# Kernel optimization log

Hardware: AMD Instinct MI355X
Metric: run time of the kernel (lower is better)

## Reference

```python
import jax, jax.numpy as jnp
import numpy as np


def setup_inputs() -> dict:
    key = jax.random.key(0)
    ks = jax.random.split(key, 4)
    B, T, D, H, E = 4, 2048, 1024, 4096, 8
    s = 0.02
    x = jax.random.normal(ks[0], (B, T, D), dtype=jnp.float32)
    Wr = jax.random.normal(ks[1], (D, E), dtype=jnp.float32) * s
    br = jnp.zeros((E,), dtype=jnp.float32)
    W1 = jax.random.normal(ks[2], (E, D, H), dtype=jnp.float32) * s
    b1 = jnp.zeros((E, H), dtype=jnp.float32)
    W2 = jax.random.normal(ks[3], (E, H, D), dtype=jnp.float32) * s
    b2 = jnp.zeros((E, D), dtype=jnp.float32)
    return {"x": x, "Wr": Wr, "br": br, "W1": W1, "b1": b1, "W2": W2, "b2": b2}


def reference(x, Wr, br, W1, b1, W2, b2):
    # Router: top-1 selection
    logits = jnp.einsum('btd,de->bte', x, Wr) + br            # [B,T,E]
    probs = jax.nn.softmax(logits, axis=-1)                   # [B,T,E]
    expert_idx = jnp.argmax(probs, axis=-1)                   # [B,T] int
    E = W1.shape[0]
    onehot = jax.nn.one_hot(expert_idx, E, dtype=x.dtype)     # [B,T,E]
    # Dense grouped-MLP over all experts, then combine with one-hot routing.
    # h: [B,E,T,H]
    h = jax.nn.relu(jnp.einsum('btd,edh->beth', x, W1) + b1[None, :, None, :])
    y = jnp.einsum('beth,ehd->betd', h, W2) + b2[None, :, None, :]  # [B,E,T,D]
    out = jnp.einsum('bte,betd->btd', onehot, y)              # [B,T,D]
    return out, probs, expert_idx
```

## Files before the change

kernel.cpp:

```cpp
#include <hip/hip_runtime.h>

#define NTOK 8192
#define DD 1024
#define HH 4096
#define EE 8
#define MAXBLK 72
#define NT1 16
#define NT2 64

typedef __attribute__((ext_vector_type(8))) short bf16x8;
typedef __attribute__((ext_vector_type(4))) float f32x4;

__device__ __forceinline__ unsigned short f2bf(float f) {
  unsigned u = __builtin_bit_cast(unsigned, f);
  u += 0x7fffu + ((u >> 16) & 1u);
  return (unsigned short)(u >> 16);
}

union Pack8 {
  unsigned short u[8];
  uint4 v;
};

__device__ __forceinline__ void gload_lds16(const void* g, void* l) {
  __builtin_amdgcn_global_load_lds(
      (const __attribute__((address_space(1))) unsigned int*)g,
      (__attribute__((address_space(3))) unsigned int*)l, 16, 0, 0);
}

__global__ __launch_bounds__(256) void k_router(
    const float* __restrict__ x, const float* __restrict__ Wr,
    const float* __restrict__ br, float* __restrict__ probs,
    float* __restrict__ idxf, int* __restrict__ idxi,
    unsigned short* __restrict__ xb) {
  const int lane = threadIdx.x & 63;
  const int token = blockIdx.x * 4 + (threadIdx.x >> 6);
  const float* xr = x + (size_t)token * DD;

  float acc[EE];
#pragma unroll
  for (int e = 0; e < EE; ++e) acc[e] = 0.f;

#pragma unroll
  for (int i = 0; i < 4; ++i) {
    const int d0 = i * 256 + lane * 4;
    const float4 xv = *reinterpret_cast<const float4*>(xr + d0);
    union { unsigned short u[4]; uint2 v; } pk;
    pk.u[0] = f2bf(xv.x); pk.u[1] = f2bf(xv.y);
    pk.u[2] = f2bf(xv.z); pk.u[3] = f2bf(xv.w);
    *reinterpret_cast<uint2*>(xb + (size_t)token * DD + d0) = pk.v;
    const float xs[4] = {xv.x, xv.y, xv.z, xv.w};
#pragma unroll
    for (int j = 0; j < 4; ++j) {
      const float xd = xs[j];
      const float4 w0 = *reinterpret_cast<const float4*>(Wr + (size_t)(d0 + j) * EE);
      const float4 w1 = *reinterpret_cast<const float4*>(Wr + (size_t)(d0 + j) * EE + 4);
      acc[0] += xd * w0.x; acc[1] += xd * w0.y; acc[2] += xd * w0.z; acc[3] += xd * w0.w;
      acc[4] += xd * w1.x; acc[5] += xd * w1.y; acc[6] += xd * w1.z; acc[7] += xd * w1.w;
    }
  }
#pragma unroll
  for (int s = 32; s > 0; s >>= 1) {
#pragma unroll
    for (int e = 0; e < EE; ++e) acc[e] += __shfl_xor(acc[e], s, 64);
  }

  float lg[EE];
#pragma unroll
  for (int e = 0; e < EE; ++e) lg[e] = acc[e] + br[e];

  int best = 0;
  float bv = lg[0];
#pragma unroll
  for (int e = 1; e < EE; ++e) {
    if (lg[e] > bv) { bv = lg[e]; best = e; }
  }
  float p[EE], s = 0.f;
#pragma unroll
  for (int e = 0; e < EE; ++e) { p[e] = expf(lg[e] - bv); s += p[e]; }
  const float inv = 1.f / s;

  if (lane == 0) {
#pragma unroll
    for (int e = 0; e < EE; ++e) probs[(size_t)token * EE + e] = p[e] * inv;
    idxf[token] = (float)best;
    idxi[token] = best;
  }
}

__global__ __launch_bounds__(512) void k_compact(const int* __restrict__ idxi,
                                                 int* __restrict__ cnt,
                                                 int* __restrict__ off,
                                                 int* __restrict__ sorted,
                                                 int* __restrict__ meta) {
  __shared__ int sidx[NTOK];
  __shared__ int scnt[EE], soff[EE];
  const int tid = threadIdx.x;
  for (int i = tid; i < NTOK; i += 512) sidx[i] = idxi[i];
  __syncthreads();
  const int w = tid >> 6, lane = tid & 63;
  if (w < EE) {
    int c = 0;
    for (int i = 0; i < NTOK / 64; ++i) {
      unsigned long long m = __ballot(sidx[i * 64 + lane] == w);
      c += __popcll(m);
    }
    if (lane == 0) scnt[w] = c;
  }
  __syncthreads();
  if (tid == 0) {
    int s = 0;
    for (int e = 0; e < EE; ++e) { soff[e] = s; s += scnt[e]; }
    int nb = 0;
    for (int e = 0; e < EE; ++e) {
      const int nmb = (scnt[e] + 127) >> 7;
      for (int m = 0; m < nmb; ++m) {
        meta[16 + nb] = e;
        meta[96 + nb] = m << 7;
        ++nb;
      }
    }
    meta[0] = nb;
  }
  __syncthreads();
  if (w < EE) {
    int base = soff[w];
    const unsigned long long ltmask = (1ull << lane) - 1ull;
    for (int i = 0; i < NTOK / 64; ++i) {
      const int tok = i * 64 + lane;
      const bool f = (sidx[tok] == w);
      unsigned long long m = __ballot(f);
      if (f) {
        int r = __popcll(m & ltmask);
        sorted[base + r] = tok;
      }
      base += __popcll(m);
    }
    if (lane == 0) { cnt[w] = scnt[w]; off[w] = soff[w]; }
  }
}

__global__ __launch_bounds__(256) void k_trcvt64(const float* __restrict__ in,
                                                 unsigned short* __restrict__ outp,
                                                 int R, int C) {
  const int e = blockIdx.z;
  const int r0 = blockIdx.y * 64, c0 = blockIdx.x * 64;
  const float* src = in + (size_t)e * R * C + (size_t)r0 * C + c0;
  unsigned short* dst = outp + (size_t)e * R * C + (size_t)c0 * R + r0;
  __shared__ unsigned short t[64 * 66];
  const int tid = threadIdx.x;
#pragma unroll
  for (int it = 0; it < 4; ++it) {
    const int r = it * 16 + (tid >> 4), c4 = (tid & 15) * 4;
    const float4 v = *reinterpret_cast<const float4*>(src + (size_t)r * C + c4);
    t[r * 66 + c4 + 0] = f2bf(v.x);
    t[r * 66 + c4 + 1] = f2bf(v.y);
    t[r * 66 + c4 + 2] = f2bf(v.z);
    t[r * 66 + c4 + 3] = f2bf(v.w);
  }
  __syncthreads();
#pragma unroll
  for (int it = 0; it < 2; ++it) {
    const int cc = it * 32 + (tid >> 3), r8 = (tid & 7) * 8;
    Pack8 p;
#pragma unroll
    for (int j = 0; j < 8; ++j) p.u[j] = t[(r8 + j) * 66 + cc];
    *reinterpret_cast<uint4*>(dst + (size_t)cc * R + r8) = p.v;
  }
}

__global__ __launch_bounds__(256) void k_gemm1n(
    const unsigned short* __restrict__ xb, const unsigned short* __restrict__ W1t,
    const float* __restrict__ b1, const int* __restrict__ meta,
    const int* __restrict__ cnt, const int* __restrict__ off,
    const int* __restrict__ sorted, unsigned short* __restrict__ h) {
  const int bid = blockIdx.x;
  if (bid >= meta[0]) return;
  const int e = meta[16 + bid];
  const int m0 = meta[96 + bid];
  const int c = cnt[e], base = off[e];
  const int n0 = blockIdx.y * 128;

  __shared__ __align__(16) unsigned short Al[2][128 * 64];
  __shared__ __align__(16) unsigned short Bl[2][128 * 64];

  const int tid = threadIdx.x, l = tid & 63, w = tid >> 6;

  const unsigned short* aptr[4];
  const unsigned short* bptr[4];
  int soff4[4];
#pragma unroll
  for (int i = 0; i < 4; ++i) {
    const int r = i * 32 + w * 8 + (l >> 3);
    const int swz = ((l & 7) ^ (r & 7)) * 8;
    int ar = m0 + r; if (ar >= c) ar = c - 1;
    const int tok = sorted[base + ar];
    aptr[i] = xb + (size_t)tok * DD + swz;
    bptr[i] = W1t + ((size_t)e * HH + n0 + r) * DD + swz;
    soff4[i] = r * 64 + (l & 7) * 8;
  }

  const int lr = l & 15, lg = l >> 4;
  const int wr = w >> 1, wc = w & 1;
  int aoff[4], boff[4], asw[4], bsw[4];
#pragma unroll
  for (int m = 0; m < 4; ++m) {
    int row = wr * 64 + m * 16 + lr;
    aoff[m] = row * 64; asw[m] = row & 7;
    row = wc * 64 + m * 16 + lr;
    boff[m] = row * 64; bsw[m] = row & 7;
  }

  f32x4 acc[4][4];
#pragma unroll
  for (int m = 0; m < 4; ++m)
#pragma unroll
    for (int n = 0; n < 4; ++n) acc[m][n] = {0.f, 0.f, 0.f, 0.f};

#pragma unroll
  for (int i = 0; i < 4; ++i) gload_lds16(aptr[i], &Al[0][soff4[i]]);
#pragma unroll
  for (int i = 0; i < 4; ++i) gload_lds16(bptr[i], &Bl[0][soff4[i]]);

  int cur = 0;
#pragma unroll 1
  for (int t = 0; t < NT1 - 1; ++t) {
    const int kn = (t + 1) * 64;
#pragma unroll
    for (int i = 0; i < 4; ++i) gload_lds16(aptr[i] + kn, &Al[cur ^ 1][soff4[i]]);
    asm volatile("s_waitcnt vmcnt(4)" ::: "memory");
    __builtin_amdgcn_s_barrier();
    {
      bf16x8 af[4], bv[4];
#pragma unroll
      for (int m = 0; m < 4; ++m)
        af[m] = *reinterpret_cast<const bf16x8*>(&Al[cur][aoff[m] + ((lg ^ asw[m]) * 8)]);
#pragma unroll
      for (int n = 0; n < 4; ++n)
        bv[n] = *reinterpret_cast<const bf16x8*>(&Bl[cur][boff[n] + ((lg ^ bsw[n]) * 8)]);
#pragma unroll
      for (int m = 0; m < 4; ++m)
#pragma unroll
        for (int n = 0; n < 4; ++n)
          acc[m][n] = __builtin_amdgcn_mfma_f32_16x16x32_bf16(af[m], bv[n], acc[m][n], 0, 0, 0);
    }
#pragma unroll
    for (int i = 0; i < 4; ++i) gload_lds16(bptr[i] + kn, &Bl[cur ^ 1][soff4[i]]);
    {
      bf16x8 af[4], bv[4];
#pragma unroll
      for (int m = 0; m < 4; ++m)
        af[m] = *reinterpret_cast<const bf16x8*>(&Al[cur][aoff[m] + (((4 + lg) ^ asw[m]) * 8)]);
#pragma unroll
      for (int n = 0; n < 4; ++n)
        bv[n] = *reinterpret_cast<const bf16x8*>(&Bl[cur][boff[n] + (((4 + lg) ^ bsw[n]) * 8)]);
#pragma unroll
      for (int m = 0; m < 4; ++m)
#pragma unroll
        for (int n = 0; n < 4; ++n)
          acc[m][n] = __builtin_amdgcn_mfma_f32_16x16x32_bf16(af[m], bv[n], acc[m][n], 0, 0, 0);
    }
    __builtin_amdgcn_s_barrier();
    cur ^= 1;
  }
  asm volatile("s_waitcnt vmcnt(0)" ::: "memory");
  __builtin_amdgcn_s_barrier();
#pragma unroll
  for (int ks = 0; ks < 2; ++ks) {
    bf16x8 af[4], bv[4];
#pragma unroll
    for (int m = 0; m < 4; ++m)
      af[m] = *reinterpret_cast<const bf16x8*>(&Al[cur][aoff[m] + (((ks * 4 + lg) ^ asw[m]) * 8)]);
#pragma unroll
    for (int n = 0; n < 4; ++n)
      bv[n] = *reinterpret_cast<const bf16x8*>(&Bl[cur][boff[n] + (((ks * 4 + lg) ^ bsw[n]) * 8)]);
#pragma unroll
    for (int m = 0; m < 4; ++m)
#pragma unroll
      for (int n = 0; n < 4; ++n)
        acc[m][n] = __builtin_amdgcn_mfma_f32_16x16x32_bf16(af[m], bv[n], acc[m][n], 0, 0, 0);
  }

  const int valid = c - m0;
#pragma unroll
  for (int m = 0; m < 4; ++m) {
#pragma unroll
    for (int rr = 0; rr < 4; ++rr) {
      const int tr = wr * 64 + m * 16 + lg * 4 + rr;
      if (tr < valid) {
        const size_t row = (size_t)(base + m0 + tr);
#pragma unroll
        for (int n = 0; n < 4; ++n) {
          const int col = n0 + wc * 64 + n * 16 + lr;
          const float v = acc[m][n][rr] + b1[e * HH + col];
          h[row * HH + col] = f2bf(fmaxf(v, 0.f));
        }
      }
    }
  }
}

__global__ __launch_bounds__(256) void k_gemm2n(
    const unsigned short* __restrict__ h, const unsigned short* __restrict__ W2t,
    const float* __restrict__ b2, const int* __restrict__ meta,
    const int* __restrict__ cnt, const int* __restrict__ off,
    const int* __restrict__ sorted, float* __restrict__ out) {
  const int bid = blockIdx.x;
  if (bid >= meta[0]) return;
  const int e = meta[16 + bid];
  const int m0 = meta[96 + bid];
  const int c = cnt[e], base = off[e];
  const int n0 = blockIdx.y * 128;

  __shared__ __align__(16) unsigned short Al[2][128 * 64];
  __shared__ __align__(16) unsigned short Bl[2][128 * 64];

  const int tid = threadIdx.x, l = tid & 63, w = tid >> 6;

  const unsigned short* aptr[4];
  const unsigned short* bptr[4];
  int soff4[4];
#pragma unroll
  for (int i = 0; i < 4; ++i) {
    const int r = i * 32 + w * 8 + (l >> 3);
    const int swz = ((l & 7) ^ (r & 7)) * 8;
    int ar = m0 + r; if (ar >= c) ar = c - 1;
    aptr[i] = h + (size_t)(base + ar) * HH + swz;
    bptr[i] = W2t + ((size_t)e * DD + n0 + r) * HH + swz;
    soff4[i] = r * 64 + (l & 7) * 8;
  }

  const int lr = l & 15, lg = l >> 4;
  const int wr = w >> 1, wc = w & 1;
  int aoff[4], boff[4], asw[4], bsw[4];
#pragma unroll
  for (int m = 0; m < 4; ++m) {
    int row = wr * 64 + m * 16 + lr;
    aoff[m] = row * 64; asw[m] = row & 7;
    row = wc * 64 + m * 16 + lr;
    boff[m] = row * 64; bsw[m] = row & 7;
  }

  f32x4 acc[4][4];
#pragma unroll
  for (int m = 0; m < 4; ++m)
#pragma unroll
    for (int n = 0; n < 4; ++n) acc[m][n] = {0.f, 0.f, 0.f, 0.f};

#pragma unroll
  for (int i = 0; i < 4; ++i) gload_lds16(aptr[i], &Al[0][soff4[i]]);
#pragma unroll
  for (int i = 0; i < 4; ++i) gload_lds16(bptr[i], &Bl[0][soff4[i]]);

  int cur = 0;
#pragma unroll 1
  for (int t = 0; t < NT2 - 1; ++t) {
    const int kn = (t + 1) * 64;
#pragma unroll
    for (int i = 0; i < 4; ++i) gload_lds16(aptr[i] + kn, &Al[cur ^ 1][soff4[i]]);
    asm volatile("s_waitcnt vmcnt(4)" ::: "memory");
    __builtin_amdgcn_s_barrier();
    {
      bf16x8 af[4], bv[4];
#pragma unroll
      for (int m = 0; m < 4; ++m)
        af[m] = *reinterpret_cast<const bf16x8*>(&Al[cur][aoff[m] + ((lg ^ asw[m]) * 8)]);
#pragma unroll
      for (int n = 0; n < 4; ++n)
        bv[n] = *reinterpret_cast<const bf16x8*>(&Bl[cur][boff[n] + ((lg ^ bsw[n]) * 8)]);
#pragma unroll
      for (int m = 0; m < 4; ++m)
#pragma unroll
        for (int n = 0; n < 4; ++n)
          acc[m][n] = __builtin_amdgcn_mfma_f32_16x16x32_bf16(af[m], bv[n], acc[m][n], 0, 0, 0);
    }
#pragma unroll
    for (int i = 0; i < 4; ++i) gload_lds16(bptr[i] + kn, &Bl[cur ^ 1][soff4[i]]);
    {
      bf16x8 af[4], bv[4];
#pragma unroll
      for (int m = 0; m < 4; ++m)
        af[m] = *reinterpret_cast<const bf16x8*>(&Al[cur][aoff[m] + (((4 + lg) ^ asw[m]) * 8)]);
#pragma unroll
      for (int n = 0; n < 4; ++n)
        bv[n] = *reinterpret_cast<const bf16x8*>(&Bl[cur][boff[n] + (((4 + lg) ^ bsw[n]) * 8)]);
#pragma unroll
      for (int m = 0; m < 4; ++m)
#pragma unroll
        for (int n = 0; n < 4; ++n)
          acc[m][n] = __builtin_amdgcn_mfma_f32_16x16x32_bf16(af[m], bv[n], acc[m][n], 0, 0, 0);
    }
    __builtin_amdgcn_s_barrier();
    cur ^= 1;
  }
  asm volatile("s_waitcnt vmcnt(0)" ::: "memory");
  __builtin_amdgcn_s_barrier();
#pragma unroll
  for (int ks = 0; ks < 2; ++ks) {
    bf16x8 af[4], bv[4];
#pragma unroll
    for (int m = 0; m < 4; ++m)
      af[m] = *reinterpret_cast<const bf16x8*>(&Al[cur][aoff[m] + (((ks * 4 + lg) ^ asw[m]) * 8)]);
#pragma unroll
    for (int n = 0; n < 4; ++n)
      bv[n] = *reinterpret_cast<const bf16x8*>(&Bl[cur][boff[n] + (((ks * 4 + lg) ^ bsw[n]) * 8)]);
#pragma unroll
    for (int m = 0; m < 4; ++m)
#pragma unroll
      for (int n = 0; n < 4; ++n)
        acc[m][n] = __builtin_amdgcn_mfma_f32_16x16x32_bf16(af[m], bv[n], acc[m][n], 0, 0, 0);
  }

  const int valid = c - m0;
#pragma unroll
  for (int m = 0; m < 4; ++m) {
#pragma unroll
    for (int rr = 0; rr < 4; ++rr) {
      const int tr = wr * 64 + m * 16 + lg * 4 + rr;
      if (tr < valid) {
        const int token = sorted[base + m0 + tr];
#pragma unroll
        for (int n = 0; n < 4; ++n) {
          const int col = n0 + wc * 64 + n * 16 + lr;
          out[(size_t)token * DD + col] = acc[m][n][rr] + b2[e * DD + col];
        }
      }
    }
  }
}

extern "C" void kernel_launch(void* const* d_in, const int* in_sizes, int n_in,
                              void* d_out, int out_size, void* d_ws, size_t ws_size,
                              hipStream_t stream) {
  const float* x  = (const float*)d_in[0];
  const float* Wr = (const float*)d_in[1];
  const float* br = (const float*)d_in[2];
  const float* W1 = (const float*)d_in[3];
  const float* b1 = (const float*)d_in[4];
  const float* W2 = (const float*)d_in[5];
  const float* b2 = (const float*)d_in[6];

  float* out   = (float*)d_out;
  float* probs = out + (size_t)NTOK * DD;
  float* idxf  = probs + (size_t)NTOK * EE;

  char* ws = (char*)d_ws;
  int* cnt    = (int*)(ws + 0);
  int* off    = (int*)(ws + 64);
  int* meta   = (int*)(ws + 128);
  int* idxi   = (int*)(ws + 1024);
  int* sorted = (int*)(ws + 33792);

  const size_t OFF_XB  = 66560;
  const size_t OFF_W1T = OFF_XB + (size_t)NTOK * DD * 2;
  const size_t OFF_H   = OFF_W1T + (size_t)EE * DD * HH * 2;
  const size_t OFF_W2T = OFF_XB;

  unsigned short* xb  = (unsigned short*)(ws + OFF_XB);
  unsigned short* W1t = (unsigned short*)(ws + OFF_W1T);
  unsigned short* W2t = (unsigned short*)(ws + OFF_W2T);
  unsigned short* h   = (unsigned short*)(ws + OFF_H);

  k_router<<<NTOK / 4, 256, 0, stream>>>(x, Wr, br, probs, idxf, idxi, xb);
  k_compact<<<1, 512, 0, stream>>>(idxi, cnt, off, sorted, meta);
  k_trcvt64<<<dim3(HH / 64, DD / 64, EE), 256, 0, stream>>>(W1, W1t, DD, HH);
  k_gemm1n<<<dim3(MAXBLK, HH / 128), 256, 0, stream>>>(xb, W1t, b1, meta, cnt, off, sorted, h);
  k_trcvt64<<<dim3(DD / 64, HH / 64, EE), 256, 0, stream>>>(W2, W2t, HH, DD);
  k_gemm2n<<<dim3(MAXBLK, DD / 128), 256, 0, stream>>>(h, W2t, b2, meta, cnt, off, sorted, out);
}
```

Before: 412.0 us.

## Split GEMM2 K-dimension across two warp groups and drop double buffering

The second expert GEMM now runs with 512 threads in two warp groups, each covering half of the H reduction with its own LDS tiles. Partial sums are combined through LDS before the output is written. Both GEMMs also drop the async double-buffered pipeline for a simpler single-buffered load, sync, compute loop. The aim is more waves per block on the small GEMM2 grid, traded against lost load/compute overlap and the cost of the extra reduction.

```diff
diff --git a/kernel.cpp b/kernel.cpp
--- a/kernel.cpp
+++ b/kernel.cpp
@@ -5,8 +5,6 @@
 #define HH 4096
 #define EE 8
 #define MAXBLK 72
-#define NT1 16
-#define NT2 64
 
 typedef __attribute__((ext_vector_type(8))) short bf16x8;
 typedef __attribute__((ext_vector_type(4))) float f32x4;
@@ -181,8 +179,8 @@
   const int c = cnt[e], base = off[e];
   const int n0 = blockIdx.y * 128;
 
-  __shared__ __align__(16) unsigned short Al[2][128 * 64];
-  __shared__ __align__(16) unsigned short Bl[2][128 * 64];
+  __shared__ __align__(16) unsigned short Al[128 * 64];
+  __shared__ __align__(16) unsigned short Bl[128 * 64];
 
   const int tid = threadIdx.x, l = tid & 63, w = tid >> 6;
 
@@ -217,68 +215,28 @@
 #pragma unroll
     for (int n = 0; n < 4; ++n) acc[m][n] = {0.f, 0.f, 0.f, 0.f};
 
-#pragma unroll
-  for (int i = 0; i < 4; ++i) gload_lds16(aptr[i], &Al[0][soff4[i]]);
-#pragma unroll
-  for (int i = 0; i < 4; ++i) gload_lds16(bptr[i], &Bl[0][soff4[i]]);
-
-  int cur = 0;
-#pragma unroll 1
-  for (int t = 0; t < NT1 - 1; ++t) {
-    const int kn = (t + 1) * 64;
-#pragma unroll
-    for (int i = 0; i < 4; ++i) gload_lds16(aptr[i] + kn, &Al[cur ^ 1][soff4[i]]);
-    asm volatile("s_waitcnt vmcnt(4)" ::: "memory");
-    __builtin_amdgcn_s_barrier();
-    {
+  for (int k0 = 0; k0 < DD; k0 += 64) {
+    __syncthreads();
+#pragma unroll
+    for (int i = 0; i < 4; ++i) gload_lds16(aptr[i] + k0, &Al[soff4[i]]);
+#pragma unroll
+    for (int i = 0; i < 4; ++i) gload_lds16(bptr[i] + k0, &Bl[soff4[i]]);
+    __syncthreads();
+#pragma unroll
+    for (int ks = 0; ks < 2; ++ks) {
       bf16x8 af[4], bv[4];
 #pragma unroll
       for (int m = 0; m < 4; ++m)
-        af[m] = *reinterpret_cast<const bf16x8*>(&Al[cur][aoff[m] + ((lg ^ asw[m]) * 8)]);
+        af[m] = *reinterpret_cast<const bf16x8*>(&Al[aoff[m] + (((ks * 4 + lg) ^ asw[m]) * 8)]);
 #pragma unroll
       for (int n = 0; n < 4; ++n)
-        bv[n] = *reinterpret_cast<const bf16x8*>(&Bl[cur][boff[n] + ((lg ^ bsw[n]) * 8)]);
+        bv[n] = *reinterpret_cast<const bf16x8*>(&Bl[boff[n] + (((ks * 4 + lg) ^ bsw[n]) * 8)]);
 #pragma unroll
       for (int m = 0; m < 4; ++m)
 #pragma unroll
         for (int n = 0; n < 4; ++n)
           acc[m][n] = __builtin_amdgcn_mfma_f32_16x16x32_bf16(af[m], bv[n], acc[m][n], 0, 0, 0);
     }
-#pragma unroll
-    for (int i = 0; i < 4; ++i) gload_lds16(bptr[i] + kn, &Bl[cur ^ 1][soff4[i]]);
-    {
-      bf16x8 af[4], bv[4];
-#pragma unroll
-      for (int m = 0; m < 4; ++m)
-        af[m] = *reinterpret_cast<const bf16x8*>(&Al[cur][aoff[m] + (((4 + lg) ^ asw[m]) * 8)]);
-#pragma unroll
-      for (int n = 0; n < 4; ++n)
-        bv[n] = *reinterpret_cast<const bf16x8*>(&Bl[cur][boff[n] + (((4 + lg) ^ bsw[n]) * 8)]);
-#pragma unroll
-      for (int m = 0; m < 4; ++m)
-#pragma unroll
-        for (int n = 0; n < 4; ++n)
-          acc[m][n] = __builtin_amdgcn_mfma_f32_16x16x32_bf16(af[m], bv[n], acc[m][n], 0, 0, 0);
-    }
-    __builtin_amdgcn_s_barrier();
-    cur ^= 1;
-  }
-  asm volatile("s_waitcnt vmcnt(0)" ::: "memory");
-  __builtin_amdgcn_s_barrier();
-#pragma unroll
-  for (int ks = 0; ks < 2; ++ks) {
-    bf16x8 af[4], bv[4];
-#pragma unroll
-    for (int m = 0; m < 4; ++m)
-      af[m] = *reinterpret_cast<const bf16x8*>(&Al[cur][aoff[m] + (((ks * 4 + lg) ^ asw[m]) * 8)]);
-#pragma unroll
-    for (int n = 0; n < 4; ++n)
-      bv[n] = *reinterpret_cast<const bf16x8*>(&Bl[cur][boff[n] + (((ks * 4 + lg) ^ bsw[n]) * 8)]);
-#pragma unroll
-    for (int m = 0; m < 4; ++m)
-#pragma unroll
-      for (int n = 0; n < 4; ++n)
-        acc[m][n] = __builtin_amdgcn_mfma_f32_16x16x32_bf16(af[m], bv[n], acc[m][n], 0, 0, 0);
   }
 
   const int valid = c - m0;
@@ -300,7 +258,7 @@
   }
 }
 
-__global__ __launch_bounds__(256) void k_gemm2n(
+__global__ __launch_bounds__(512) void k_gemm2s(
     const unsigned short* __restrict__ h, const unsigned short* __restrict__ W2t,
     const float* __restrict__ b2, const int* __restrict__ meta,
     const int* __restrict__ cnt, const int* __restrict__ off,
@@ -312,26 +270,28 @@
   const int c = cnt[e], base = off[e];
   const int n0 = blockIdx.y * 128;
 
-  __shared__ __align__(16) unsigned short Al[2][128 * 64];
-  __shared__ __align__(16) unsigned short Bl[2][128 * 64];
-
-  const int tid = threadIdx.x, l = tid & 63, w = tid >> 6;
+  __shared__ __align__(16) unsigned short LDSU[4][128 * 64];
+
+  const int tid = threadIdx.x, l = tid & 63;
+  const int w = tid >> 6;
+  const int g = w >> 2;
+  const int wg = w & 3;
 
   const unsigned short* aptr[4];
   const unsigned short* bptr[4];
   int soff4[4];
 #pragma unroll
   for (int i = 0; i < 4; ++i) {
-    const int r = i * 32 + w * 8 + (l >> 3);
+    const int r = i * 32 + wg * 8 + (l >> 3);
     const int swz = ((l & 7) ^ (r & 7)) * 8;
     int ar = m0 + r; if (ar >= c) ar = c - 1;
-    aptr[i] = h + (size_t)(base + ar) * HH + swz;
-    bptr[i] = W2t + ((size_t)e * DD + n0 + r) * HH + swz;
+    aptr[i] = h + (size_t)(base + ar) * HH + g * 2048 + swz;
+    bptr[i] = W2t + ((size_t)e * DD + n0 + r) * HH + g * 2048 + swz;
     soff4[i] = r * 64 + (l & 7) * 8;
   }
 
   const int lr = l & 15, lg = l >> 4;
-  const int wr = w >> 1, wc = w & 1;
+  const int wr = wg >> 1, wc = wg & 1;
   int aoff[4], boff[4], asw[4], bsw[4];
 #pragma unroll
   for (int m = 0; m < 4; ++m) {
@@ -347,82 +307,62 @@
 #pragma unroll
     for (int n = 0; n < 4; ++n) acc[m][n] = {0.f, 0.f, 0.f, 0.f};
 
-#pragma unroll
-  for (int i = 0; i < 4; ++i) gload_lds16(aptr[i], &Al[0][soff4[i]]);
-#pragma unroll
-  for (int i = 0; i < 4; ++i) gload_lds16(bptr[i], &Bl[0][soff4[i]]);
-
-  int cur = 0;
-#pragma unroll 1
-  for (int t = 0; t < NT2 - 1; ++t) {
-    const int kn = (t + 1) * 64;
-#pragma unroll
-    for (int i = 0; i < 4; ++i) gload_lds16(aptr[i] + kn, &Al[cur ^ 1][soff4[i]]);
-    asm volatile("s_waitcnt vmcnt(4)" ::: "memory");
-    __builtin_amdgcn_s_barrier();
-    {
+  for (int t = 0; t < 32; ++t) {
+    const int k0 = t * 64;
+    __syncthreads();
+#pragma unroll
+    for (int i = 0; i < 4; ++i) gload_lds16(aptr[i] + k0, &LDSU[g][soff4[i]]);
+#pragma unroll
+    for (int i = 0; i < 4; ++i) gload_lds16(bptr[i] + k0, &LDSU[2 + g][soff4[i]]);
+    __syncthreads();
+#pragma unroll
+    for (int ks = 0; ks < 2; ++ks) {
       bf16x8 af[4], bv[4];
 #pragma unroll
       for (int m = 0; m < 4; ++m)
-        af[m] = *reinterpret_cast<const bf16x8*>(&Al[cur][aoff[m] + ((lg ^ asw[m]) * 8)]);
+        af[m] = *reinterpret_cast<const bf16x8*>(&LDSU[g][aoff[m] + (((ks * 4 + lg) ^ asw[m]) * 8)]);
 #pragma unroll
       for (int n = 0; n < 4; ++n)
-        bv[n] = *reinterpret_cast<const bf16x8*>(&Bl[cur][boff[n] + ((lg ^ bsw[n]) * 8)]);
+        bv[n] = *reinterpret_cast<const bf16x8*>(&LDSU[2 + g][boff[n] + (((ks * 4 + lg) ^ bsw[n]) * 8)]);
 #pragma unroll
       for (int m = 0; m < 4; ++m)
 #pragma unroll
         for (int n = 0; n < 4; ++n)
           acc[m][n] = __builtin_amdgcn_mfma_f32_16x16x32_bf16(af[m], bv[n], acc[m][n], 0, 0, 0);
     }
-#pragma unroll
-    for (int i = 0; i < 4; ++i) gload_lds16(bptr[i] + kn, &Bl[cur ^ 1][soff4[i]]);
-    {
-      bf16x8 af[4], bv[4];
-#pragma unroll
-      for (int m = 0; m < 4; ++m)
-        af[m] = *reinterpret_cast<const bf16x8*>(&Al[cur][aoff[m] + (((4 + lg) ^ asw[m]) * 8)]);
-#pragma unroll
-      for (int n = 0; n < 4; ++n)
-        bv[n] = *reinterpret_cast<const bf16x8*>(&Bl[cur][boff[n] + (((4 + lg) ^ bsw[n]) * 8)]);
-#pragma unroll
-      for (int m = 0; m < 4; ++m)
-#pragma unroll
-        for (int n = 0; n < 4; ++n)
-          acc[m][n] = __builtin_amdgcn_mfma_f32_16x16x32_bf16(af[m], bv[n], acc[m][n], 0, 0, 0);
-    }
-    __builtin_amdgcn_s_barrier();
-    cur ^= 1;
-  }
-  asm volatile("s_waitcnt vmcnt(0)" ::: "memory");
-  __builtin_amdgcn_s_barrier();
-#pragma unroll
-  for (int ks = 0; ks < 2; ++ks) {
-    bf16x8 af[4], bv[4];
+  }
+
+  __syncthreads();
+  float* red = (float*)LDSU;
+  if (g == 1) {
 #pragma unroll
     for (int m = 0; m < 4; ++m)
-      af[m] = *reinterpret_cast<const bf16x8*>(&Al[cur][aoff[m] + (((ks * 4 + lg) ^ asw[m]) * 8)]);
-#pragma unroll
-    for (int n = 0; n < 4; ++n)
-      bv[n] = *reinterpret_cast<const bf16x8*>(&Bl[cur][boff[n] + (((ks * 4 + lg) ^ bsw[n]) * 8)]);
-#pragma unroll
-    for (int m = 0; m < 4; ++m)
-#pragma unroll
-      for (int n = 0; n < 4; ++n)
-        acc[m][n] = __builtin_amdgcn_mfma_f32_16x16x32_bf16(af[m], bv[n], acc[m][n], 0, 0, 0);
-  }
-
-  const int valid = c - m0;
-#pragma unroll
-  for (int m = 0; m < 4; ++m) {
-#pragma unroll
-    for (int rr = 0; rr < 4; ++rr) {
-      const int tr = wr * 64 + m * 16 + lg * 4 + rr;
-      if (tr < valid) {
-        const int token = sorted[base + m0 + tr];
+#pragma unroll
+      for (int rr = 0; rr < 4; ++rr) {
+        const int row = wr * 64 + m * 16 + lg * 4 + rr;
 #pragma unroll
         for (int n = 0; n < 4; ++n) {
-          const int col = n0 + wc * 64 + n * 16 + lr;
-          out[(size_t)token * DD + col] = acc[m][n][rr] + b2[e * DD + col];
+          const int col = wc * 64 + n * 16 + lr;
+          red[row * 128 + col] = acc[m][n][rr];
+        }
+      }
+  }
+  __syncthreads();
+  if (g == 0) {
+    const int valid = c - m0;
+#pragma unroll
+    for (int m = 0; m < 4; ++m) {
+#pragma unroll
+      for (int rr = 0; rr < 4; ++rr) {
+        const int tr = wr * 64 + m * 16 + lg * 4 + rr;
+        if (tr < valid) {
+          const int token = sorted[base + m0 + tr];
+#pragma unroll
+          for (int n = 0; n < 4; ++n) {
+            const int col = wc * 64 + n * 16 + lr;
+            out[(size_t)token * DD + n0 + col] =
+                acc[m][n][rr] + red[tr * 128 + col] + b2[e * DD + n0 + col];
+          }
         }
       }
     }
@@ -466,5 +406,5 @@
   k_trcvt64<<<dim3(HH / 64, DD / 64, EE), 256, 0, stream>>>(W1, W1t, DD, HH);
   k_gemm1n<<<dim3(MAXBLK, HH / 128), 256, 0, stream>>>(xb, W1t, b1, meta, cnt, off, sorted, h);
   k_trcvt64<<<dim3(DD / 64, HH / 64, EE), 256, 0, stream>>>(W2, W2t, HH, DD);
-  k_gemm2n<<<dim3(MAXBLK, DD / 128), 256, 0, stream>>>(h, W2t, b2, meta, cnt, off, sorted, out);
-}
+  k_gemm2s<<<dim3(MAXBLK, DD / 128), 512, 0, stream>>>(h, W2t, b2, meta, cnt, off, sorted, out);
+}
```

Result: faster. 400.3 us (-2.9%).
